# Optimization experiments

Hardware: AMD Instinct MI355X
Metric: run time of the kernel (lower is better)

## Reference

```python
import jax, jax.numpy as jnp
import numpy as np
import math

D_MODEL = 1024
NUM_HEADS = 16
HEAD_DIM = D_MODEL // NUM_HEADS
WINDOW = 5  # positions j with i - W//2 <= j <= i + W//2 are visible


def setup_inputs() -> dict:
    key = jax.random.key(0)
    ks = jax.random.split(key, 9)
    B, S = 2, 2048
    x = jax.random.normal(ks[0], (B, S, D_MODEL), dtype=jnp.float32)
    # Xavier-uniform linear weights [out, in] (torch convention), zero biases
    lim = math.sqrt(6.0 / (D_MODEL + D_MODEL))
    def w(k):
        return jax.random.uniform(k, (D_MODEL, D_MODEL), dtype=jnp.float32, minval=-lim, maxval=lim)
    return {
        'x': x,
        'Wq': w(ks[1]), 'bq': jnp.zeros((D_MODEL,), jnp.float32),
        'Wk': w(ks[2]), 'bk': jnp.zeros((D_MODEL,), jnp.float32),
        'Wv': w(ks[3]), 'bv': jnp.zeros((D_MODEL,), jnp.float32),
        'Wo': w(ks[4]), 'bo': jnp.zeros((D_MODEL,), jnp.float32),
    }


def reference(x, Wq, bq, Wk, bk, Wv, bv, Wo, bo):
    B, S, D = x.shape
    H, hd = NUM_HEADS, HEAD_DIM
    half = WINDOW // 2

    def proj(W, b):
        # torch Linear: y = x @ W.T + b ; split heads -> [B, H, S, hd]
        return (jnp.einsum('bsd,ed->bse', x, W) + b).reshape(B, S, H, hd).transpose(0, 2, 1, 3)

    q = proj(Wq, bq)
    k = proj(Wk, bk)
    v = proj(Wv, bv)

    scores = jnp.einsum('bhqd,bhkd->bhqk', q, k) / jnp.sqrt(jnp.asarray(hd, x.dtype))
    i = jnp.arange(S)[:, None]
    j = jnp.arange(S)[None, :]
    band = (j >= i - half) & (j <= i + half)  # [S, S] local window mask
    scores = jnp.where(band, scores, jnp.asarray(-1e9, x.dtype))
    attn = jax.nn.softmax(scores, axis=-1)  # dropout is identity in eval mode
    out = jnp.einsum('bhqk,bhkd->bhqd', attn, v)
    out = out.transpose(0, 2, 1, 3).reshape(B, S, D)
    return jnp.einsum('bsd,ed->bse', out, Wo) + bo
```

## Files before the change

### kernel.cpp

```cpp
#include <hip/hip_runtime.h>
#include <hip/hip_bf16.h>

typedef __bf16 bf16_t;
typedef __bf16 bf16x4 __attribute__((ext_vector_type(4)));
typedef __bf16 bf16x8 __attribute__((ext_vector_type(8)));
typedef float f32x4 __attribute__((ext_vector_type(4)));

#define S_LEN 2048
#define DMODEL 1024
#define NHEADS 16
#define HDIM 64
#define BROWS 4096

__device__ __forceinline__ void async16(const void* g, void* l) {
  __builtin_amdgcn_global_load_lds(
      (const __attribute__((address_space(1))) void*)g,
      (__attribute__((address_space(3))) void*)l, 16, 0, 0);
}

__global__ __launch_bounds__(256) void cvt_all_kernel(
    const float* __restrict__ x, const float* __restrict__ Wq,
    const float* __restrict__ Wk, const float* __restrict__ Wv,
    const float* __restrict__ Wo, bf16_t* __restrict__ dst) {
  const int i = blockIdx.x * 256 + threadIdx.x;
  constexpr int XN4 = (BROWS * DMODEL) / 4;
  constexpr int WN4 = (DMODEL * DMODEL) / 4;
  const float* src;
  size_t off;
  if (i < XN4) {
    src = x;
    off = (size_t)i;
  } else {
    const int wi = i - XN4;
    const int w = wi >> 18;
    off = (size_t)(wi & (WN4 - 1));
    src = (w == 0) ? Wq : (w == 1) ? Wk : (w == 2) ? Wv : Wo;
  }
  const float4 v = *(const float4*)(src + off * 4);
  bf16x4 o;
  o[0] = (bf16_t)v.x;
  o[1] = (bf16_t)v.y;
  o[2] = (bf16_t)v.z;
  o[3] = (bf16_t)v.w;
  *(bf16x4*)(dst + (size_t)i * 4) = o;
}

template <typename OutT>
__device__ __forceinline__ void gemm_body(
    const bf16_t* __restrict__ A, const bf16_t* __restrict__ W,
    const float* __restrict__ bias, OutT* __restrict__ C, int m0, int n0) {
  constexpr int Kd = 1024, Nd = 1024, BK = 32, NT = Kd / BK;
  __shared__ bf16_t ldsA[2][128 * BK];
  __shared__ bf16_t ldsB[2][128 * BK];

  const int tid = threadIdx.x;
  const int lane = tid & 63;
  const int wave = tid >> 6;
  const int wr = wave >> 1;
  const int wc = wave & 1;

  f32x4 acc[4][4] = {};

  const int fr = lane & 15;
  const int ko = (lane >> 4) * 8;

  auto stage = [&](int buf, int t) {
    const int k0 = t * BK;
#pragma unroll
    for (int p = 0; p < 2; ++p) {
      const int off = (p * 256 + tid) * 16;
      const int row = off >> 6;
      const int kb = off & 63;
      async16((const char*)(A + (size_t)(m0 + row) * Kd + k0) + kb,
              (char*)ldsA[buf] + off);
      async16((const char*)(W + (size_t)(n0 + row) * Kd + k0) + kb,
              (char*)ldsB[buf] + off);
    }
  };

  auto compute = [&](int buf) {
    bf16x8 af[4], bfr[4];
#pragma unroll
    for (int i = 0; i < 4; ++i)
      af[i] = *(const bf16x8*)(ldsA[buf] + (wr * 64 + i * 16 + fr) * BK + ko);
#pragma unroll
    for (int j = 0; j < 4; ++j)
      bfr[j] = *(const bf16x8*)(ldsB[buf] + (wc * 64 + j * 16 + fr) * BK + ko);
#pragma unroll
    for (int i = 0; i < 4; ++i)
#pragma unroll
      for (int j = 0; j < 4; ++j)
        acc[i][j] = __builtin_amdgcn_mfma_f32_16x16x32_bf16(af[i], bfr[j],
                                                            acc[i][j], 0, 0, 0);
  };

  stage(0, 0);
  __syncthreads();
#pragma unroll 1
  for (int t = 0; t < NT; ++t) {
    if (t + 1 < NT) stage((t + 1) & 1, t + 1);
    compute(t & 1);
    __syncthreads();
  }

  const int cr = (lane >> 4) * 4;
#pragma unroll
  for (int j = 0; j < 4; ++j) {
    const int col = n0 + wc * 64 + j * 16 + fr;
    const float bv = bias[col];
#pragma unroll
    for (int i = 0; i < 4; ++i) {
#pragma unroll
      for (int r = 0; r < 4; ++r) {
        const int row = m0 + wr * 64 + i * 16 + cr + r;
        C[(size_t)row * Nd + col] = (OutT)(acc[i][j][r] + bv);
      }
    }
  }
}

__global__ __launch_bounds__(256) void gemm_qkv_kernel(
    const bf16_t* __restrict__ xb, const bf16_t* __restrict__ Wqb,
    const bf16_t* __restrict__ Wkb, const bf16_t* __restrict__ Wvb,
    const float* __restrict__ bq, const float* __restrict__ bk,
    const float* __restrict__ bv, bf16_t* __restrict__ Q,
    bf16_t* __restrict__ K, bf16_t* __restrict__ V) {
  const int mat = blockIdx.y >> 3;
  const int nt = blockIdx.y & 7;
  const bf16_t* W = (mat == 0) ? Wqb : (mat == 1) ? Wkb : Wvb;
  const float* bias = (mat == 0) ? bq : (mat == 1) ? bk : bv;
  bf16_t* C = (mat == 0) ? Q : (mat == 1) ? K : V;
  gemm_body<bf16_t>(xb, W, bias, C, blockIdx.x * 128, nt * 128);
}

__global__ __launch_bounds__(256) void gemm_o_kernel(
    const bf16_t* __restrict__ ctx, const bf16_t* __restrict__ Wob,
    const float* __restrict__ bo, float* __restrict__ out) {
  gemm_body<float>(ctx, Wob, bo, out, blockIdx.x * 128, blockIdx.y * 128);
}

#define CHUNK 256
#define TROWS 260

__global__ __launch_bounds__(256) void attn_kernel(
    const bf16_t* __restrict__ Q, const bf16_t* __restrict__ K,
    const bf16_t* __restrict__ V, bf16_t* __restrict__ ctx) {
  __shared__ bf16_t ldsK[TROWS * HDIM];
  __shared__ bf16_t ldsV[TROWS * HDIM];

  const int tid = threadIdx.x;
  const int blk = blockIdx.x;
  const int chunk = blk & 7;
  const int bh = blk >> 3;
  const int h = bh & (NHEADS - 1);
  const int b = bh >> 4;
  const int s0 = chunk * CHUNK;

  const bf16_t* Kb = K + (size_t)b * S_LEN * DMODEL + h * HDIM;
  const bf16_t* Vb = V + (size_t)b * S_LEN * DMODEL + h * HDIM;

#pragma unroll
  for (int j = 0; j < 9; ++j) {
    const int i = j * 256 + tid;
    if (i < TROWS * 8) {
      const int tr = i >> 3;
      const int slot = i & 7;
      const int c = slot ^ (tr & 7);
      int gs = s0 - 2 + tr;
      gs = (gs < 0) ? 0 : (gs >= S_LEN ? S_LEN - 1 : gs);
      async16((const char*)(Kb + (size_t)gs * DMODEL) + c * 16,
              (char*)ldsK + i * 16);
      async16((const char*)(Vb + (size_t)gs * DMODEL) + c * 16,
              (char*)ldsV + i * 16);
    }
  }

  const int s = s0 + tid;
  const bf16_t* Qrow = Q + ((size_t)(b * S_LEN) + s) * DMODEL + h * HDIM;
  bf16x8 q8[8];
#pragma unroll
  for (int c = 0; c < 8; ++c) q8[c] = *(const bf16x8*)(Qrow + c * 8);
  float qf[64];
#pragma unroll
  for (int c = 0; c < 8; ++c)
#pragma unroll
    for (int e = 0; e < 8; ++e) qf[c * 8 + e] = (float)q8[c][e];

  __syncthreads();

  float sc[5];
#pragma unroll
  for (int jj = 0; jj < 5; ++jj) {
    const int tr = tid + jj;
    float d = 0.f;
#pragma unroll
    for (int c = 0; c < 8; ++c) {
      const bf16x8 k8 =
          *(const bf16x8*)(ldsK + tr * HDIM + (c ^ (tr & 7)) * 8);
#pragma unroll
      for (int e = 0; e < 8; ++e) d += qf[c * 8 + e] * (float)k8[e];
    }
    const int j = s - 2 + jj;
    sc[jj] = (j < 0 || j >= S_LEN) ? -1e30f : d * 0.125f;
  }

  float m = sc[0];
#pragma unroll
  for (int jj = 1; jj < 5; ++jj) m = fmaxf(m, sc[jj]);
  float p[5], l = 0.f;
#pragma unroll
  for (int jj = 0; jj < 5; ++jj) {
    p[jj] = __expf(sc[jj] - m);
    l += p[jj];
  }
  const float inv = 1.0f / l;
#pragma unroll
  for (int jj = 0; jj < 5; ++jj) p[jj] *= inv;

  float o[64];
#pragma unroll
  for (int e = 0; e < 64; ++e) o[e] = 0.f;
#pragma unroll
  for (int jj = 0; jj < 5; ++jj) {
    const int tr = tid + jj;
    const float pj = p[jj];
#pragma unroll
    for (int c = 0; c < 8; ++c) {
      const bf16x8 v8 =
          *(const bf16x8*)(ldsV + tr * HDIM + (c ^ (tr & 7)) * 8);
#pragma unroll
      for (int e = 0; e < 8; ++e) o[c * 8 + e] += pj * (float)v8[e];
    }
  }

  bf16_t* Crow = (bf16_t*)ctx + ((size_t)(b * S_LEN) + s) * DMODEL + h * HDIM;
#pragma unroll
  for (int c = 0; c < 8; ++c) {
    bf16x8 ov;
#pragma unroll
    for (int e = 0; e < 8; ++e) ov[e] = (bf16_t)o[c * 8 + e];
    *(bf16x8*)(Crow + c * 8) = ov;
  }
}

extern "C" void kernel_launch(void* const* d_in, const int* in_sizes, int n_in,
                              void* d_out, int out_size, void* d_ws,
                              size_t ws_size, hipStream_t stream) {
  const float* x = (const float*)d_in[0];
  const float* Wq = (const float*)d_in[1];
  const float* bq = (const float*)d_in[2];
  const float* Wk = (const float*)d_in[3];
  const float* bk = (const float*)d_in[4];
  const float* Wv = (const float*)d_in[5];
  const float* bv = (const float*)d_in[6];
  const float* Wo = (const float*)d_in[7];
  const float* bo = (const float*)d_in[8];
  float* out = (float*)d_out;

  const size_t mat = (size_t)BROWS * DMODEL;
  const size_t wmat = (size_t)DMODEL * DMODEL;
  bf16_t* xb = (bf16_t*)d_ws;
  bf16_t* Wqb = xb + mat;
  bf16_t* Wkb = Wqb + wmat;
  bf16_t* Wvb = Wkb + wmat;
  bf16_t* Wob = Wvb + wmat;
  bf16_t* Q = Wob + wmat;
  bf16_t* K = Q + mat;
  bf16_t* V = K + mat;
  bf16_t* ctx = V + mat;

  cvt_all_kernel<<<8192, 256, 0, stream>>>(x, Wq, Wk, Wv, Wo, xb);

  gemm_qkv_kernel<<<dim3(32, 24), 256, 0, stream>>>(xb, Wqb, Wkb, Wvb, bq, bk,
                                                    bv, Q, K, V);
  attn_kernel<<<256, 256, 0, stream>>>(Q, K, V, ctx);
  gemm_o_kernel<<<dim3(32, 8), 256, 0, stream>>>(ctx, Wob, bo, out);
}
```

Measured before the change: 80.19 us.

## Replace QKV GEMM with 256x256-tile, 8-wave pipelined kernel

The QKV projection GEMM moves from 128x128 tiles with 4 waves to 256x256 tiles with 8 waves and BK=64. It uses a hand-scheduled double-buffered pipeline with XOR-swizzled LDS, explicit vmcnt/lgkmcnt waits, barriers and setprio around the MFMA clusters. The aim is more data reuse per tile and better overlap of global loads with MFMA work. The trade-off is a 128KB LDS footprint and only 192 blocks, which may underfill the 256 CUs, plus fragile hand-tuned synchronisation.

```diff
diff --git a/kernel.cpp b/kernel.cpp
--- a/kernel.cpp
+++ b/kernel.cpp
@@ -45,6 +45,186 @@
   *(bf16x4*)(dst + (size_t)i * 4) = o;
 }
 
+#define BARR __builtin_amdgcn_s_barrier()
+#define LGKM0 asm volatile("s_waitcnt lgkmcnt(0)" ::: "memory")
+#define VMC4 asm volatile("s_waitcnt vmcnt(4)" ::: "memory")
+#define VMC0 asm volatile("s_waitcnt vmcnt(0)" ::: "memory")
+
+template <typename OutT>
+__device__ __forceinline__ void gemm256_body(
+    const bf16_t* __restrict__ A, const bf16_t* __restrict__ W,
+    const float* __restrict__ bias, OutT* __restrict__ C, int m0, int n0,
+    char* lds) {
+  constexpr int Kd = 1024, Nd = 1024;
+  char* ldsA = lds;
+  char* ldsB = lds + 65536;
+
+  const int tid = threadIdx.x;
+  const int lane = tid & 63;
+  const int wid = tid >> 6;
+  const int wr = wid >> 2;
+  const int wc = wid & 3;
+  const int fr = lane & 15;
+  const int l16 = lane >> 4;
+
+  f32x4 acc[8][4] = {};
+  bf16x8 aA[4][2], bB[4][2];
+
+  auto stage = [&](const bf16_t* G, char* ldsX, int gr0, int buf, int h,
+                   int kt) {
+#pragma unroll
+    for (int l = 0; l < 2; ++l) {
+      const int idx = l * 512 + tid;
+      const int r = idx >> 3;
+      const int slot = idx & 7;
+      async16((const char*)(G + (size_t)(gr0 + h * 128 + r) * Kd + kt * 64 +
+                            ((slot ^ (r & 7)) << 3)),
+              ldsX + buf * 32768 + h * 16384 + r * 128 + slot * 16);
+    }
+  };
+
+  auto rdA = [&](int buf, int row, int ks) -> bf16x8 {
+    return *(const bf16x8*)(ldsA + buf * 32768 + row * 128 +
+                            ((((ks << 2) + l16) ^ (row & 7)) << 4));
+  };
+  auto rdB = [&](int buf, int row, int ks) -> bf16x8 {
+    return *(const bf16x8*)(ldsB + buf * 32768 + row * 128 +
+                            ((((ks << 2) + l16) ^ (row & 7)) << 4));
+  };
+
+#define RDA(MH, BUF)                                          \
+  _Pragma("unroll") for (int m_ = 0; m_ < 4; ++m_)            \
+      _Pragma("unroll") for (int ks_ = 0; ks_ < 2; ++ks_)     \
+          aA[m_][ks_] = rdA(BUF, wr * 128 + (MH)*64 + m_ * 16 + fr, ks_);
+#define RDB(NH, BUF)                                          \
+  _Pragma("unroll") for (int n_ = 0; n_ < 2; ++n_)            \
+      _Pragma("unroll") for (int ks_ = 0; ks_ < 2; ++ks_)     \
+          bB[(NH)*2 + n_][ks_] = rdB(BUF, wc * 64 + (NH)*32 + n_ * 16 + fr, ks_);
+#define MMAQ(MH, NH)                                                          \
+  _Pragma("unroll") for (int m_ = 0; m_ < 4; ++m_)                            \
+      _Pragma("unroll") for (int n_ = 0; n_ < 2; ++n_) {                      \
+    acc[(MH)*4 + m_][(NH)*2 + n_] = __builtin_amdgcn_mfma_f32_16x16x32_bf16(  \
+        aA[m_][0], bB[(NH)*2 + n_][0], acc[(MH)*4 + m_][(NH)*2 + n_], 0, 0,   \
+        0);                                                                   \
+    acc[(MH)*4 + m_][(NH)*2 + n_] = __builtin_amdgcn_mfma_f32_16x16x32_bf16(  \
+        aA[m_][1], bB[(NH)*2 + n_][1], acc[(MH)*4 + m_][(NH)*2 + n_], 0, 0,   \
+        0);                                                                   \
+  }
+
+  stage(A, ldsA, m0, 0, 0, 0);
+  stage(A, ldsA, m0, 0, 1, 0);
+  stage(W, ldsB, n0, 0, 0, 0);
+  stage(W, ldsB, n0, 0, 1, 0);
+  stage(W, ldsB, n0, 1, 0, 1);
+  stage(W, ldsB, n0, 1, 1, 1);
+  VMC4;
+  BARR;
+
+#pragma unroll 1
+  for (int i = 0; i < 8; ++i) {
+    const int t0 = 2 * i, t1 = 2 * i + 1;
+    const bool st = (i < 7);
+    RDA(0, 0);
+    RDB(0, 0);
+    stage(A, ldsA, m0, 1, 0, t1);
+    BARR;
+    LGKM0;
+    __builtin_amdgcn_s_setprio(1);
+    MMAQ(0, 0);
+    __builtin_amdgcn_s_setprio(0);
+    BARR;
+    RDB(1, 0);
+    stage(A, ldsA, m0, 1, 1, t1);
+    BARR;
+    LGKM0;
+    __builtin_amdgcn_s_setprio(1);
+    MMAQ(0, 1);
+    __builtin_amdgcn_s_setprio(0);
+    BARR;
+    RDA(1, 0);
+    if (st) stage(W, ldsB, n0, 0, 0, t0 + 2);
+    BARR;
+    LGKM0;
+    __builtin_amdgcn_s_setprio(1);
+    MMAQ(1, 0);
+    __builtin_amdgcn_s_setprio(0);
+    BARR;
+    if (st) stage(W, ldsB, n0, 0, 1, t0 + 2);
+    __builtin_amdgcn_s_setprio(1);
+    MMAQ(1, 1);
+    __builtin_amdgcn_s_setprio(0);
+    if (st) {
+      VMC4;
+    } else {
+      VMC0;
+    }
+    BARR;
+    RDA(0, 1);
+    RDB(0, 1);
+    if (st) stage(A, ldsA, m0, 0, 0, t0 + 2);
+    BARR;
+    LGKM0;
+    __builtin_amdgcn_s_setprio(1);
+    MMAQ(0, 0);
+    __builtin_amdgcn_s_setprio(0);
+    BARR;
+    RDB(1, 1);
+    if (st) stage(A, ldsA, m0, 0, 1, t0 + 2);
+    BARR;
+    LGKM0;
+    __builtin_amdgcn_s_setprio(1);
+    MMAQ(0, 1);
+    __builtin_amdgcn_s_setprio(0);
+    BARR;
+    RDA(1, 1);
+    if (st) stage(W, ldsB, n0, 1, 0, t1 + 2);
+    BARR;
+    LGKM0;
+    __builtin_amdgcn_s_setprio(1);
+    MMAQ(1, 0);
+    __builtin_amdgcn_s_setprio(0);
+    BARR;
+    if (st) stage(W, ldsB, n0, 1, 1, t1 + 2);
+    __builtin_amdgcn_s_setprio(1);
+    MMAQ(1, 1);
+    __builtin_amdgcn_s_setprio(0);
+    if (st) VMC4;
+    BARR;
+  }
+#undef RDA
+#undef RDB
+#undef MMAQ
+
+  const int cr = l16 * 4;
+#pragma unroll
+  for (int nf = 0; nf < 4; ++nf) {
+    const int col = n0 + wc * 64 + nf * 16 + fr;
+    const float bv = bias[col];
+#pragma unroll
+    for (int mf = 0; mf < 8; ++mf) {
+      const int row = m0 + wr * 128 + mf * 16 + cr;
+#pragma unroll
+      for (int r = 0; r < 4; ++r)
+        C[(size_t)(row + r) * Nd + col] = (OutT)(acc[mf][nf][r] + bv);
+    }
+  }
+}
+
+__global__ __launch_bounds__(512, 2) void gemm_qkv256_kernel(
+    const bf16_t* __restrict__ xb, const bf16_t* __restrict__ Wqkv,
+    const float* __restrict__ bq, const float* __restrict__ bk,
+    const float* __restrict__ bv, bf16_t* __restrict__ Q,
+    bf16_t* __restrict__ K, bf16_t* __restrict__ V) {
+  __shared__ char lds[131072];
+  const int nt = blockIdx.y;
+  const int mat = nt >> 2;
+  const int n0 = (nt & 3) * 256;
+  const bf16_t* W = Wqkv + (size_t)mat * DMODEL * DMODEL;
+  const float* bias = (mat == 0) ? bq : (mat == 1) ? bk : bv;
+  bf16_t* C = (mat == 0) ? Q : (mat == 1) ? K : V;
+  gemm256_body<bf16_t>(xb, W, bias, C, blockIdx.x * 256, n0, lds);
+}
+
 template <typename OutT>
 __device__ __forceinline__ void gemm_body(
     const bf16_t* __restrict__ A, const bf16_t* __restrict__ W,
@@ -117,20 +297,6 @@
       }
     }
   }
-}
-
-__global__ __launch_bounds__(256) void gemm_qkv_kernel(
-    const bf16_t* __restrict__ xb, const bf16_t* __restrict__ Wqb,
-    const bf16_t* __restrict__ Wkb, const bf16_t* __restrict__ Wvb,
-    const float* __restrict__ bq, const float* __restrict__ bk,
-    const float* __restrict__ bv, bf16_t* __restrict__ Q,
-    bf16_t* __restrict__ K, bf16_t* __restrict__ V) {
-  const int mat = blockIdx.y >> 3;
-  const int nt = blockIdx.y & 7;
-  const bf16_t* W = (mat == 0) ? Wqb : (mat == 1) ? Wkb : Wvb;
-  const float* bias = (mat == 0) ? bq : (mat == 1) ? bk : bv;
-  bf16_t* C = (mat == 0) ? Q : (mat == 1) ? K : V;
-  gemm_body<bf16_t>(xb, W, bias, C, blockIdx.x * 128, nt * 128);
 }
 
 __global__ __launch_bounds__(256) void gemm_o_kernel(
@@ -195,8 +361,7 @@
     float d = 0.f;
 #pragma unroll
     for (int c = 0; c < 8; ++c) {
-      const bf16x8 k8 =
-          *(const bf16x8*)(ldsK + tr * HDIM + (c ^ (tr & 7)) * 8);
+      const bf16x8 k8 = *(const bf16x8*)(ldsK + tr * HDIM + (c ^ (tr & 7)) * 8);
 #pragma unroll
       for (int e = 0; e < 8; ++e) d += qf[c * 8 + e] * (float)k8[e];
     }
@@ -226,8 +391,7 @@
     const float pj = p[jj];
 #pragma unroll
     for (int c = 0; c < 8; ++c) {
-      const bf16x8 v8 =
-          *(const bf16x8*)(ldsV + tr * HDIM + (c ^ (tr & 7)) * 8);
+      const bf16x8 v8 = *(const bf16x8*)(ldsV + tr * HDIM + (c ^ (tr & 7)) * 8);
 #pragma unroll
       for (int e = 0; e < 8; ++e) o[c * 8 + e] += pj * (float)v8[e];
     }
@@ -261,9 +425,7 @@
   const size_t wmat = (size_t)DMODEL * DMODEL;
   bf16_t* xb = (bf16_t*)d_ws;
   bf16_t* Wqb = xb + mat;
-  bf16_t* Wkb = Wqb + wmat;
-  bf16_t* Wvb = Wkb + wmat;
-  bf16_t* Wob = Wvb + wmat;
+  bf16_t* Wob = Wqb + 3 * wmat;
   bf16_t* Q = Wob + wmat;
   bf16_t* K = Q + mat;
   bf16_t* V = K + mat;
@@ -271,8 +433,8 @@
 
   cvt_all_kernel<<<8192, 256, 0, stream>>>(x, Wq, Wk, Wv, Wo, xb);
 
-  gemm_qkv_kernel<<<dim3(32, 24), 256, 0, stream>>>(xb, Wqb, Wkb, Wvb, bq, bk,
-                                                    bv, Q, K, V);
+  gemm_qkv256_kernel<<<dim3(16, 12), 512, 0, stream>>>(xb, Wqb, bq, bk, bv, Q,
+                                                       K, V);
   attn_kernel<<<256, 256, 0, stream>>>(Q, K, V, ctx);
   gemm_o_kernel<<<dim3(32, 8), 256, 0, stream>>>(ctx, Wob, bo, out);
 }
```

Result: no change. 80.67 us (+0.6%).
